# Performance work log

Measured on AMD Instinct MI355X. Metric: run time of the kernel, lower is better.

Reference implementation:

```python
import jax, jax.numpy as jnp
import numpy as np

H = 8  # n_heads

def setup_inputs() -> dict:
    key = jax.random.key(0)
    ks = jax.random.split(key, 7)
    B, G, D, KD, E = 16, 1024, 512, 64, 512  # batch, graph_size, input_dim, key_dim=embed//H, embed_dim
    q = jax.random.normal(ks[0], (B * G, D), jnp.float32)
    mask = jax.random.bernoulli(ks[1], 0.15, (B, G))  # True = padded node
    s_in = 1.0 / np.sqrt(D)
    Wq = jax.random.uniform(ks[2], (KD, D), jnp.float32, -s_in, s_in)
    Wk = jax.random.uniform(ks[3], (KD, D), jnp.float32, -s_in, s_in)
    Wv = jax.random.uniform(ks[4], (KD, D), jnp.float32, -s_in, s_in)
    s_o = 1.0 / np.sqrt(KD)
    Wout_w = jax.random.uniform(ks[5], (E, KD), jnp.float32, -s_o, s_o)
    Wout_b = jax.random.uniform(ks[6], (E,), jnp.float32, -1.0 / np.sqrt(E), 1.0 / np.sqrt(E))
    return {"q": q, "mask": mask, "Wq": Wq, "Wk": Wk, "Wv": Wv,
            "Wout_w": Wout_w, "Wout_b": Wout_b, "graph_size": G}


def reference(q, mask, Wq, Wk, Wv, Wout_w, Wout_b, graph_size):
    G = graph_size
    B = q.shape[0] // G
    KD = Wq.shape[0]
    norm = 1.0 / jnp.sqrt(jnp.asarray(KD, jnp.float32))
    # torch .view(n_heads, B, G, -1) on a (B*G, KD) tensor: row-major reshape
    Q = (q @ Wq.T).reshape(H, B, G, -1)  # per-head dim = KD // H
    K = (q @ Wk.T).reshape(H, B, G, -1)
    V = (q @ Wv.T).reshape(H, B, G, -1)
    compat = norm * jnp.einsum('hbqd,hbkd->hbqk', Q, K)  # (H,B,G,G)
    m = mask[None, :, None, :]  # broadcast == repeat over query dim and heads
    compat = jnp.where(m, jnp.float32(-30.0), compat)  # evaluate=False path
    attn = jax.nn.softmax(compat, axis=-1)
    attn = jnp.where(m, jnp.float32(0.0), attn)  # second mask fill
    heads = jnp.einsum('hbqk,hbkd->hbqd', attn, V)  # (H,B,G,KD//H)
    # permute(1,2,0,3) then flatten heads -> (B*G, H*(KD//H)=KD)
    out = heads.transpose(1, 2, 0, 3).reshape(B * G, -1) @ Wout_w.T + Wout_b
    return out
```

## Files before the change

### kernel.cpp

```cpp
#include <hip/hip_runtime.h>
#include <hip/hip_bf16.h>

#define NROWS 16384
#define DDIM  512
#define KDIM  64
#define EDIM  512
#define GSZ   1024
#define BSZ   16
#define HSZ   8

typedef float f32x16 __attribute__((ext_vector_type(16)));
typedef short bf16x8 __attribute__((ext_vector_type(8)));

union FragU { uint u[4]; uint4 u4; bf16x8 s; };

static __device__ __forceinline__ float fexp2(float x) {
  return __builtin_amdgcn_exp2f(x);
}
static __device__ __forceinline__ uint bf16r(float x) {
  const uint u = __builtin_bit_cast(uint, x);
  return (u + 0x7FFFu + ((u >> 16) & 1u)) >> 16;
}
static __device__ __forceinline__ uint apk(float lo, float hi) {
  uint r;
  asm("v_cvt_pk_bf16_f32 %0, %1, %2" : "=v"(r) : "v"(lo), "v"(hi));
  return r;
}
static __device__ __forceinline__ uint pk2e(float a, float b) {
  const uint lo = __builtin_bit_cast(uint, fexp2(a)) + 0x8000u;
  const uint hi = __builtin_bit_cast(uint, fexp2(b)) + 0x8000u;
  return __builtin_amdgcn_perm(hi, lo, 0x07060302u);
}
static __device__ __forceinline__ void plswap(uint& a, uint& b) {
  auto r = __builtin_amdgcn_permlane32_swap(a, b, false, false);
  a = r[0]; b = r[1];
}
static __device__ __forceinline__ void plswapf(float& a, float& b) {
  uint au = __builtin_bit_cast(uint, a), bu = __builtin_bit_cast(uint, b);
  plswap(au, bu);
  a = __builtin_bit_cast(float, au); b = __builtin_bit_cast(float, bu);
}
static __device__ __forceinline__ uint vperm16(uint a, uint b, int d1) {
  const uint lo = d1 ? (a >> 16) : (a & 0xFFFFu);
  const uint hi = d1 ? (b >> 16) : (b & 0xFFFFu);
  return lo | (hi << 16);
}

__global__ __launch_bounds__(256) void k_mask3(const void* __restrict__ mraw,
                                               uint* __restrict__ onesw,
                                               uint* __restrict__ vmw) {
  __shared__ int flags[2];
  const int tid = threadIdx.x;
  if (tid < 2) flags[tid] = 0;
  __syncthreads();
  const unsigned int* u = (const unsigned int*)mraw;
  int bad = 0, isf = 0;
  for (int i = tid; i < 4096; i += 256) {
    const unsigned v = u[i];
    bad |= (v > 1u) ? 1 : 0;
    isf |= (v == 0x3F800000u) ? 1 : 0;
  }
  if (bad) flags[0] = 1;
  if (isf) flags[1] = 1;
  __syncthreads();
  const int fmt = flags[1] ? 2 : (flags[0] ? 1 : 0);
  const int b = blockIdx.x;
  for (int pair = tid; pair < 512; pair += 256) {
    const int g0 = b * GSZ + pair * 2;
    bool m0, m1;
    if (fmt == 0) {
      m0 = ((const int*)mraw)[g0] != 0;  m1 = ((const int*)mraw)[g0 + 1] != 0;
    } else if (fmt == 1) {
      m0 = ((const unsigned char*)mraw)[g0] != 0;
      m1 = ((const unsigned char*)mraw)[g0 + 1] != 0;
    } else {
      m0 = ((const float*)mraw)[g0] != 0.0f;
      m1 = ((const float*)mraw)[g0 + 1] != 0.0f;
    }
    onesw[b * 512 + pair] = (m0 ? 0u : 0x3F80u) | (m1 ? 0u : 0x3F800000u);
    vmw[b * 512 + pair]   = (m0 ? 0u : 0xFFFFu) | (m1 ? 0u : 0xFFFF0000u);
  }
}

__global__ __launch_bounds__(384) void k_qkv2(const float* __restrict__ q,
    const float* __restrict__ Wq, const float* __restrict__ Wk,
    const float* __restrict__ Wv,
    ushort* __restrict__ Qbf, ushort* __restrict__ Kbf, ushort* __restrict__ Vbf) {
  __shared__ uint4 lds_a[16 * 64];
  __shared__ uint4 lds_w[16 * 192];
  const int tid = threadIdx.x;
  const int rowbase = blockIdx.x * 64;
  const int w = tid >> 6, lane = tid & 63, hi = lane >> 5, ln = lane & 31;
  const int wr = (w < 3) ? 0 : 1;
  const int wc = (w < 3) ? w : (w - 3);

  f32x16 acc0, acc1;
#pragma unroll
  for (int j = 0; j < 16; ++j) { acc0[j] = 0.0f; acc1[j] = 0.0f; }

#pragma unroll 1
  for (int ch = 0; ch < 4; ++ch) {
    const int k0 = ch * 128;
    __syncthreads();
#pragma unroll 1
    for (int ep = tid; ep < 512; ep += 384) {
      const int row = ep >> 3, sp = ep & 7;
      const float* src = q + (size_t)(rowbase + row) * DDIM + k0 + sp * 16;
      const float4 f0 = *(const float4*)(src);
      const float4 f1 = *(const float4*)(src + 4);
      const float4 f2 = *(const float4*)(src + 8);
      const float4 f3 = *(const float4*)(src + 12);
      uint4 w0, w1;
      w0.x = apk(f0.x, f0.y); w0.y = apk(f0.z, f0.w);
      w0.z = apk(f1.x, f1.y); w0.w = apk(f1.z, f1.w);
      w1.x = apk(f2.x, f2.y); w1.y = apk(f2.z, f2.w);
      w1.z = apk(f3.x, f3.y); w1.w = apk(f3.z, f3.w);
      const int sl0 = sp * 2, sl1 = sp * 2 + 1;
      lds_a[sl0 * 64 + (row ^ (sl0 & 7))] = w0;
      lds_a[sl1 * 64 + (row ^ (sl1 & 7))] = w1;
    }
#pragma unroll 1
    for (int ep = tid; ep < 1536; ep += 384) {
      const int c = ep >> 3, sp = ep & 7;
      const float* wsrc = (c < 64) ? (Wq + (size_t)c * DDIM)
                        : (c < 128) ? (Wk + (size_t)(c - 64) * DDIM)
                                    : (Wv + (size_t)(c - 128) * DDIM);
      const float* src = wsrc + k0 + sp * 16;
      const float4 f0 = *(const float4*)(src);
      const float4 f1 = *(const float4*)(src + 4);
      const float4 f2 = *(const float4*)(src + 8);
      const float4 f3 = *(const float4*)(src + 12);
      uint4 w0, w1;
      w0.x = apk(f0.x, f0.y); w0.y = apk(f0.z, f0.w);
      w0.z = apk(f1.x, f1.y); w0.w = apk(f1.z, f1.w);
      w1.x = apk(f2.x, f2.y); w1.y = apk(f2.z, f2.w);
      w1.z = apk(f3.x, f3.y); w1.w = apk(f3.z, f3.w);
      const int sl0 = sp * 2, sl1 = sp * 2 + 1;
      lds_w[sl0 * 192 + (c ^ (sl0 & 7))] = w0;
      lds_w[sl1 * 192 + (c ^ (sl1 & 7))] = w1;
    }
    __syncthreads();
#pragma unroll
    for (int kc8 = 0; kc8 < 8; ++kc8) {
      const int sl = kc8 * 2 + hi;
      FragU aq, b0, b1;
      aq.u4 = lds_a[sl * 64 + ((wr * 32 + ln) ^ (sl & 7))];
      b0.u4 = lds_w[sl * 192 + ((wc * 64 + ln) ^ (sl & 7))];
      b1.u4 = lds_w[sl * 192 + ((wc * 64 + 32 + ln) ^ (sl & 7))];
      acc0 = __builtin_amdgcn_mfma_f32_32x32x16_bf16(aq.s, b0.s, acc0, 0, 0, 0);
      acc1 = __builtin_amdgcn_mfma_f32_32x32x16_bf16(aq.s, b1.s, acc1, 0, 0, 0);
    }
  }

  constexpr float QS = 0.125f * 1.44269504088896340736f;
  ushort* dst = (wc == 0) ? Qbf : (wc == 1) ? Kbf : Vbf;
  const float scale = (wc == 0) ? QS : 1.0f;
#pragma unroll
  for (int j = 0; j < 16; ++j) {
    const int row = rowbase + wr * 32 + (j & 3) + 8 * (j >> 2) + 4 * hi;
    dst[(size_t)row * 64 + ln]      = (ushort)bf16r(acc0[j] * scale);
    dst[(size_t)row * 64 + 32 + ln] = (ushort)bf16r(acc1[j] * scale);
  }
}

__global__ __launch_bounds__(256) void k_attn7(const ushort* __restrict__ Qbf,
    const ushort* __restrict__ Kbf, const ushort* __restrict__ Vbf,
    const uint* __restrict__ onesw, const uint* __restrict__ vmw,
    float* __restrict__ Hm) {
  __shared__ __align__(16) uint4  KL[1025];
  __shared__ __align__(16) ushort VT[9 * 1040];
  const int tid = threadIdx.x;
  const int b = blockIdx.y, h = blockIdx.z;
  const size_t hb = ((size_t)h * 2048 + (size_t)b * 128) * 64;

#pragma unroll
  for (int i = 0; i < 4; ++i) {
    const int tt = tid + i * 256;
    KL[tt] = *(const uint4*)(&Kbf[hb + (size_t)tt * 8]);
  }
  if (tid == 0) {
    uint4 z; z.x = 0; z.y = 0; z.z = 0; z.w = 0;
    KL[1024] = z;
  }
#pragma unroll
  for (int i = 0; i < 2; ++i) {
    const int pair = tid + i * 256;
    const int t = pair * 2;
    const uint ow = onesw[b * 512 + pair];
    const uint vm = vmw[b * 512 + pair];
    const uint4 v0 = *(const uint4*)(&Vbf[hb + (size_t)t * 8]);
    const uint4 v1 = *(const uint4*)(&Vbf[hb + (size_t)(t + 1) * 8]);
    const uint* ap = (const uint*)&v0;
    const uint* cp = (const uint*)&v1;
    const int s = t & 15;
    const int c = (t & ~15) | (s & 3) | ((s & 4) << 1) | ((s & 8) >> 1);
#pragma unroll
    for (int d = 0; d < 8; ++d)
      *(uint*)&VT[d * 1040 + c] = vperm16(ap[d >> 1], cp[d >> 1], d & 1) & vm;
    *(uint*)&VT[8 * 1040 + c] = ow;
  }

  const int w = tid >> 6, lane = tid & 63, hi = lane >> 5, ln = lane & 31;
  const int q = (blockIdx.x * 4 + w) * 32 + ln;

  FragU bq;
  bq.u4 = *(const uint4*)(&Qbf[hb + (size_t)q * 8]);
  __syncthreads();

  f32x16 acc;
#pragma unroll
  for (int j = 0; j < 16; ++j) acc[j] = 0.0f;
  f32x16 zero;
#pragma unroll
  for (int j = 0; j < 16; ++j) zero[j] = 0.0f;

  const char* kptr = (const char*)KL + (hi ? 1024 * 16 : ln * 16);
  const int kstep = hi ? 0 : 512;
  const ushort* vptr = VT + (ln < 8 ? ln : 8) * 1040 + hi * 8;

#pragma unroll 2
  for (int kt = 0; kt < 32; ++kt) {
    FragU ka, va0, va1;
    ka.u4  = *(const uint4*)kptr;
    va0.u4 = *(const uint4*)(vptr);
    va1.u4 = *(const uint4*)(vptr + 16);
    kptr += kstep;
    vptr += 32;

    f32x16 s = __builtin_amdgcn_mfma_f32_32x32x16_bf16(ka.s, bq.s, zero, 0, 0, 0);

    FragU pa, pb;
    pa.u[0] = pk2e(s[0], s[1]);   pa.u[1] = pk2e(s[2], s[3]);
    pa.u[2] = pk2e(s[4], s[5]);   pa.u[3] = pk2e(s[6], s[7]);
    pb.u[0] = pk2e(s[8], s[9]);   pb.u[1] = pk2e(s[10], s[11]);
    pb.u[2] = pk2e(s[12], s[13]); pb.u[3] = pk2e(s[14], s[15]);

    acc = __builtin_amdgcn_mfma_f32_32x32x16_bf16(va0.s, pa.s, acc, 0, 0, 0);
    acc = __builtin_amdgcn_mfma_f32_32x32x16_bf16(va1.s, pb.s, acc, 0, 0, 0);
  }

  float la = acc[4], lb = acc[4];
  plswapf(la, lb);
  const float inv = (la > 0.0f) ? 1.0f / la : 0.0f;
  float* op = Hm + ((size_t)b * GSZ + q) * 64 + h * 8 + hi * 4;
  *(float4*)op = make_float4(acc[0] * inv, acc[1] * inv, acc[2] * inv, acc[3] * inv);
}

__global__ __launch_bounds__(256) void k_out2(const float* __restrict__ Hm,
    const float* __restrict__ Ww, const float* __restrict__ Wb,
    float* __restrict__ out) {
  __shared__ uint4 lds_h[8 * 128];
  __shared__ uint4 lds_e[8 * 128];
  const int tid = threadIdx.x;
  const int colbase = blockIdx.x * 128;
  const int rowbase = blockIdx.y * 128;
  const int w = tid >> 6, lane = tid & 63, hi = lane >> 5, ln = lane & 31;
  const int wr = w >> 1, wc = w & 1;

#pragma unroll
  for (int i = 0; i < 2; ++i) {
    const int ep = tid + i * 256;
    const int row = ep >> 2, sp = ep & 3;
    const float* src = Hm + (size_t)(rowbase + row) * 64 + sp * 16;
    const float4 f0 = *(const float4*)(src);
    const float4 f1 = *(const float4*)(src + 4);
    const float4 f2 = *(const float4*)(src + 8);
    const float4 f3 = *(const float4*)(src + 12);
    uint4 w0, w1;
    w0.x = apk(f0.x, f0.y); w0.y = apk(f0.z, f0.w);
    w0.z = apk(f1.x, f1.y); w0.w = apk(f1.z, f1.w);
    w1.x = apk(f2.x, f2.y); w1.y = apk(f2.z, f2.w);
    w1.z = apk(f3.x, f3.y); w1.w = apk(f3.z, f3.w);
    const int sl0 = sp * 2, sl1 = sp * 2 + 1;
    lds_h[sl0 * 128 + (row ^ (sl0 & 7))] = w0;
    lds_h[sl1 * 128 + (row ^ (sl1 & 7))] = w1;
  }
#pragma unroll
  for (int i = 0; i < 2; ++i) {
    const int ep = tid + i * 256;
    const int c = ep >> 2, sp = ep & 3;
    const float* src = Ww + (size_t)(colbase + c) * 64 + sp * 16;
    const float4 f0 = *(const float4*)(src);
    const float4 f1 = *(const float4*)(src + 4);
    const float4 f2 = *(const float4*)(src + 8);
    const float4 f3 = *(const float4*)(src + 12);
    uint4 w0, w1;
    w0.x = apk(f0.x, f0.y); w0.y = apk(f0.z, f0.w);
    w0.z = apk(f1.x, f1.y); w0.w = apk(f1.z, f1.w);
    w1.x = apk(f2.x, f2.y); w1.y = apk(f2.z, f2.w);
    w1.z = apk(f3.x, f3.y); w1.w = apk(f3.z, f3.w);
    const int sl0 = sp * 2, sl1 = sp * 2 + 1;
    lds_e[sl0 * 128 + (c ^ (sl0 & 7))] = w0;
    lds_e[sl1 * 128 + (c ^ (sl1 & 7))] = w1;
  }
  __syncthreads();

  f32x16 a00, a01, a10, a11;
#pragma unroll
  for (int j = 0; j < 16; ++j) { a00[j] = 0.0f; a01[j] = 0.0f; a10[j] = 0.0f; a11[j] = 0.0f; }

#pragma unroll
  for (int kc8 = 0; kc8 < 4; ++kc8) {
    const int sl = kc8 * 2 + hi;
    FragU fa0, fa1, fb0, fb1;
    fa0.u4 = lds_h[sl * 128 + ((wr * 64 + ln) ^ (sl & 7))];
    fa1.u4 = lds_h[sl * 128 + ((wr * 64 + 32 + ln) ^ (sl & 7))];
    fb0.u4 = lds_e[sl * 128 + ((wc * 64 + ln) ^ (sl & 7))];
    fb1.u4 = lds_e[sl * 128 + ((wc * 64 + 32 + ln) ^ (sl & 7))];
    a00 = __builtin_amdgcn_mfma_f32_32x32x16_bf16(fa0.s, fb0.s, a00, 0, 0, 0);
    a01 = __builtin_amdgcn_mfma_f32_32x32x16_bf16(fa0.s, fb1.s, a01, 0, 0, 0);
    a10 = __builtin_amdgcn_mfma_f32_32x32x16_bf16(fa1.s, fb0.s, a10, 0, 0, 0);
    a11 = __builtin_amdgcn_mfma_f32_32x32x16_bf16(fa1.s, fb1.s, a11, 0, 0, 0);
  }

  const float bias0 = Wb[colbase + wc * 64 + ln];
  const float bias1 = Wb[colbase + wc * 64 + 32 + ln];
  const int col0 = colbase + wc * 64 + ln;
#pragma unroll
  for (int j = 0; j < 16; ++j) {
    const int r0 = rowbase + wr * 64 + (j & 3) + 8 * (j >> 2) + 4 * hi;
    out[(size_t)r0 * EDIM + col0]            = a00[j] + bias0;
    out[(size_t)r0 * EDIM + col0 + 32]       = a01[j] + bias1;
    out[(size_t)(r0 + 32) * EDIM + col0]      = a10[j] + bias0;
    out[(size_t)(r0 + 32) * EDIM + col0 + 32] = a11[j] + bias1;
  }
}

extern "C" void kernel_launch(void* const* d_in, const int* in_sizes, int n_in,
                              void* d_out, int out_size, void* d_ws, size_t ws_size,
                              hipStream_t stream) {
  const float* q    = (const float*)d_in[0];
  const void*  mask = d_in[1];
  const float* Wq   = (const float*)d_in[2];
  const float* Wk   = (const float*)d_in[3];
  const float* Wv   = (const float*)d_in[4];
  const float* Ww   = (const float*)d_in[5];
  const float* Wb   = (const float*)d_in[6];

  float* ws = (float*)d_ws;
  float* Hm    = ws;
  uint*  onesw = (uint*)(Hm + (size_t)NROWS * KDIM);
  uint*  vmw   = onesw + BSZ * 512;
  ushort* Qbf  = (ushort*)(vmw + BSZ * 512);
  ushort* Kbf  = Qbf + (size_t)NROWS * KDIM;
  ushort* Vbf  = Kbf + (size_t)NROWS * KDIM;

  k_mask3<<<BSZ, 256, 0, stream>>>(mask, onesw, vmw);
  k_qkv2<<<NROWS / 64, 384, 0, stream>>>(q, Wq, Wk, Wv, Qbf, Kbf, Vbf);
  k_attn7<<<dim3(8, BSZ, HSZ), 256, 0, stream>>>(Qbf, Kbf, Vbf, onesw, vmw, Hm);
  k_out2<<<dim3(EDIM / 128, NROWS / 128), 256, 0, stream>>>(Hm, Ww, Wb, (float*)d_out);
}
```

Baseline: 62.63 us.

## Split attention keys into two shards with combine kernel; widen QKV projection blocks

The attention kernel now splits the 1024 keys into two shards per block, doubling the grid to 2048 blocks and halving per-block LDS. Each shard writes unnormalized partial outputs and row sums to a workspace, and a new combine kernel adds them and normalizes. Separately, the QKV projection uses 768 threads (12 waves, one 32x32 tile each) instead of 384 with two tiles per wave. Together these aim to raise occupancy and parallelism, at the cost of an extra kernel launch and extra global traffic for the partial results.

```diff
diff --git a/kernel.cpp b/kernel.cpp
--- a/kernel.cpp
+++ b/kernel.cpp
@@ -30,15 +30,6 @@
   const uint lo = __builtin_bit_cast(uint, fexp2(a)) + 0x8000u;
   const uint hi = __builtin_bit_cast(uint, fexp2(b)) + 0x8000u;
   return __builtin_amdgcn_perm(hi, lo, 0x07060302u);
-}
-static __device__ __forceinline__ void plswap(uint& a, uint& b) {
-  auto r = __builtin_amdgcn_permlane32_swap(a, b, false, false);
-  a = r[0]; b = r[1];
-}
-static __device__ __forceinline__ void plswapf(float& a, float& b) {
-  uint au = __builtin_bit_cast(uint, a), bu = __builtin_bit_cast(uint, b);
-  plswap(au, bu);
-  a = __builtin_bit_cast(float, au); b = __builtin_bit_cast(float, bu);
 }
 static __device__ __forceinline__ uint vperm16(uint a, uint b, int d1) {
   const uint lo = d1 ? (a >> 16) : (a & 0xFFFFu);
@@ -82,7 +73,7 @@
   }
 }
 
-__global__ __launch_bounds__(384) void k_qkv2(const float* __restrict__ q,
+__global__ __launch_bounds__(768) void k_qkv3(const float* __restrict__ q,
     const float* __restrict__ Wq, const float* __restrict__ Wk,
     const float* __restrict__ Wv,
     ushort* __restrict__ Qbf, ushort* __restrict__ Kbf, ushort* __restrict__ Vbf) {
@@ -91,19 +82,19 @@
   const int tid = threadIdx.x;
   const int rowbase = blockIdx.x * 64;
   const int w = tid >> 6, lane = tid & 63, hi = lane >> 5, ln = lane & 31;
-  const int wr = (w < 3) ? 0 : 1;
-  const int wc = (w < 3) ? w : (w - 3);
-
-  f32x16 acc0, acc1;
-#pragma unroll
-  for (int j = 0; j < 16; ++j) { acc0[j] = 0.0f; acc1[j] = 0.0f; }
+  const int wr = (w < 6) ? 0 : 1;
+  const int wc = (w < 6) ? w : (w - 6);
+
+  f32x16 acc;
+#pragma unroll
+  for (int j = 0; j < 16; ++j) acc[j] = 0.0f;
 
 #pragma unroll 1
   for (int ch = 0; ch < 4; ++ch) {
     const int k0 = ch * 128;
     __syncthreads();
 #pragma unroll 1
-    for (int ep = tid; ep < 512; ep += 384) {
+    for (int ep = tid; ep < 512; ep += 768) {
       const int row = ep >> 3, sp = ep & 7;
       const float* src = q + (size_t)(rowbase + row) * DDIM + k0 + sp * 16;
       const float4 f0 = *(const float4*)(src);
@@ -120,7 +111,7 @@
       lds_a[sl1 * 64 + (row ^ (sl1 & 7))] = w1;
     }
 #pragma unroll 1
-    for (int ep = tid; ep < 1536; ep += 384) {
+    for (int ep = tid; ep < 1536; ep += 768) {
       const int c = ep >> 3, sp = ep & 7;
       const float* wsrc = (c < 64) ? (Wq + (size_t)c * DDIM)
                         : (c < 128) ? (Wk + (size_t)(c - 64) * DDIM)
@@ -143,65 +134,64 @@
 #pragma unroll
     for (int kc8 = 0; kc8 < 8; ++kc8) {
       const int sl = kc8 * 2 + hi;
-      FragU aq, b0, b1;
+      FragU aq, bw;
       aq.u4 = lds_a[sl * 64 + ((wr * 32 + ln) ^ (sl & 7))];
-      b0.u4 = lds_w[sl * 192 + ((wc * 64 + ln) ^ (sl & 7))];
-      b1.u4 = lds_w[sl * 192 + ((wc * 64 + 32 + ln) ^ (sl & 7))];
-      acc0 = __builtin_amdgcn_mfma_f32_32x32x16_bf16(aq.s, b0.s, acc0, 0, 0, 0);
-      acc1 = __builtin_amdgcn_mfma_f32_32x32x16_bf16(aq.s, b1.s, acc1, 0, 0, 0);
+      bw.u4 = lds_w[sl * 192 + ((wc * 32 + ln) ^ (sl & 7))];
+      acc = __builtin_amdgcn_mfma_f32_32x32x16_bf16(aq.s, bw.s, acc, 0, 0, 0);
     }
   }
 
   constexpr float QS = 0.125f * 1.44269504088896340736f;
-  ushort* dst = (wc == 0) ? Qbf : (wc == 1) ? Kbf : Vbf;
-  const float scale = (wc == 0) ? QS : 1.0f;
+  ushort* dst = (wc < 2) ? Qbf : (wc < 4) ? Kbf : Vbf;
+  const int colb = (wc < 2) ? wc * 32 : (wc < 4) ? (wc - 2) * 32 : (wc - 4) * 32;
+  const float scale = (wc < 2) ? QS : 1.0f;
 #pragma unroll
   for (int j = 0; j < 16; ++j) {
     const int row = rowbase + wr * 32 + (j & 3) + 8 * (j >> 2) + 4 * hi;
-    dst[(size_t)row * 64 + ln]      = (ushort)bf16r(acc0[j] * scale);
-    dst[(size_t)row * 64 + 32 + ln] = (ushort)bf16r(acc1[j] * scale);
-  }
-}
-
-__global__ __launch_bounds__(256) void k_attn7(const ushort* __restrict__ Qbf,
+    dst[(size_t)row * 64 + colb + ln] = (ushort)bf16r(acc[j] * scale);
+  }
+}
+
+__global__ __launch_bounds__(256) void k_attn8(const ushort* __restrict__ Qbf,
     const ushort* __restrict__ Kbf, const ushort* __restrict__ Vbf,
     const uint* __restrict__ onesw, const uint* __restrict__ vmw,
-    float* __restrict__ Hm) {
-  __shared__ __align__(16) uint4  KL[1025];
-  __shared__ __align__(16) ushort VT[9 * 1040];
+    float* __restrict__ part) {
+  __shared__ __align__(16) uint4  KL[513];
+  __shared__ __align__(16) ushort VT[9 * 528];
   const int tid = threadIdx.x;
+  const int qt4 = blockIdx.x >> 1, shard = blockIdx.x & 1;
   const int b = blockIdx.y, h = blockIdx.z;
   const size_t hb = ((size_t)h * 2048 + (size_t)b * 128) * 64;
-
-#pragma unroll
-  for (int i = 0; i < 4; ++i) {
+  const int kt0 = shard * 512;
+
+#pragma unroll
+  for (int i = 0; i < 2; ++i) {
     const int tt = tid + i * 256;
-    KL[tt] = *(const uint4*)(&Kbf[hb + (size_t)tt * 8]);
+    KL[tt] = *(const uint4*)(&Kbf[hb + (size_t)(kt0 + tt) * 8]);
   }
   if (tid == 0) {
     uint4 z; z.x = 0; z.y = 0; z.z = 0; z.w = 0;
-    KL[1024] = z;
-  }
-#pragma unroll
-  for (int i = 0; i < 2; ++i) {
-    const int pair = tid + i * 256;
+    KL[512] = z;
+  }
+  {
+    const int pair = tid;
     const int t = pair * 2;
-    const uint ow = onesw[b * 512 + pair];
-    const uint vm = vmw[b * 512 + pair];
-    const uint4 v0 = *(const uint4*)(&Vbf[hb + (size_t)t * 8]);
-    const uint4 v1 = *(const uint4*)(&Vbf[hb + (size_t)(t + 1) * 8]);
+    const uint ow = onesw[b * 512 + shard * 256 + pair];
+    const uint vm = vmw[b * 512 + shard * 256 + pair];
+    const uint4 v0 = *(const uint4*)(&Vbf[hb + (size_t)(kt0 + t) * 8]);
+    const uint4 v1 = *(const uint4*)(&Vbf[hb + (size_t)(kt0 + t + 1) * 8]);
     const uint* ap = (const uint*)&v0;
     const uint* cp = (const uint*)&v1;
     const int s = t & 15;
     const int c = (t & ~15) | (s & 3) | ((s & 4) << 1) | ((s & 8) >> 1);
 #pragma unroll
     for (int d = 0; d < 8; ++d)
-      *(uint*)&VT[d * 1040 + c] = vperm16(ap[d >> 1], cp[d >> 1], d & 1) & vm;
-    *(uint*)&VT[8 * 1040 + c] = ow;
+      *(uint*)&VT[d * 528 + c] = vperm16(ap[d >> 1], cp[d >> 1], d & 1) & vm;
+    *(uint*)&VT[8 * 528 + c] = ow;
   }
 
   const int w = tid >> 6, lane = tid & 63, hi = lane >> 5, ln = lane & 31;
-  const int q = (blockIdx.x * 4 + w) * 32 + ln;
+  const int q = (qt4 * 4 + w) * 32 + ln;
 
   FragU bq;
   bq.u4 = *(const uint4*)(&Qbf[hb + (size_t)q * 8]);
@@ -214,12 +204,12 @@
 #pragma unroll
   for (int j = 0; j < 16; ++j) zero[j] = 0.0f;
 
-  const char* kptr = (const char*)KL + (hi ? 1024 * 16 : ln * 16);
+  const char* kptr = (const char*)KL + (hi ? 512 * 16 : ln * 16);
   const int kstep = hi ? 0 : 512;
-  const ushort* vptr = VT + (ln < 8 ? ln : 8) * 1040 + hi * 8;
+  const ushort* vptr = VT + (ln < 8 ? ln : 8) * 528 + hi * 8;
 
 #pragma unroll 2
-  for (int kt = 0; kt < 32; ++kt) {
+  for (int kt = 0; kt < 16; ++kt) {
     FragU ka, va0, va1;
     ka.u4  = *(const uint4*)kptr;
     va0.u4 = *(const uint4*)(vptr);
@@ -239,11 +229,32 @@
     acc = __builtin_amdgcn_mfma_f32_32x32x16_bf16(va1.s, pb.s, acc, 0, 0, 0);
   }
 
-  float la = acc[4], lb = acc[4];
-  plswapf(la, lb);
-  const float inv = (la > 0.0f) ? 1.0f / la : 0.0f;
-  float* op = Hm + ((size_t)b * GSZ + q) * 64 + h * 8 + hi * 4;
-  *(float4*)op = make_float4(acc[0] * inv, acc[1] * inv, acc[2] * inv, acc[3] * inv);
+  const size_t eidx = (((size_t)shard * BSZ + b) * GSZ + q) * HSZ + h;
+  float* ap2 = part + eidx * 8 + hi * 4;
+  *(float4*)ap2 = make_float4(acc[0], acc[1], acc[2], acc[3]);
+  if (hi == 0) {
+    float* lbase = part + (size_t)2 * BSZ * GSZ * HSZ * 8;
+    lbase[eidx] = acc[4];
+  }
+}
+
+__global__ __launch_bounds__(256) void k_comb2(const float* __restrict__ part,
+                                               float* __restrict__ Hm) {
+  const int gid = blockIdx.x * 256 + threadIdx.x;
+  const size_t sstride = (size_t)BSZ * GSZ * HSZ;
+  const float* a1 = part + (size_t)gid * 8;
+  const float* a2 = part + ((size_t)gid + sstride) * 8;
+  const float* lbase = part + 2 * sstride * 8;
+  const float l = lbase[gid] + lbase[gid + sstride];
+  const float inv = (l > 0.0f) ? 1.0f / l : 0.0f;
+  const float4 x1 = *(const float4*)a1, y1 = *(const float4*)(a1 + 4);
+  const float4 x2 = *(const float4*)a2, y2 = *(const float4*)(a2 + 4);
+  const int b = gid >> 13, q = (gid >> 3) & 1023, h = gid & 7;
+  float* op = Hm + ((size_t)b * GSZ + q) * 64 + h * 8;
+  *(float4*)op = make_float4((x1.x + x2.x) * inv, (x1.y + x2.y) * inv,
+                             (x1.z + x2.z) * inv, (x1.w + x2.w) * inv);
+  *(float4*)(op + 4) = make_float4((y1.x + y2.x) * inv, (y1.y + y2.y) * inv,
+                                   (y1.z + y2.z) * inv, (y1.w + y2.w) * inv);
 }
 
 __global__ __launch_bounds__(256) void k_out2(const float* __restrict__ Hm,
@@ -344,9 +355,11 @@
   ushort* Qbf  = (ushort*)(vmw + BSZ * 512);
   ushort* Kbf  = Qbf + (size_t)NROWS * KDIM;
   ushort* Vbf  = Kbf + (size_t)NROWS * KDIM;
+  float* part  = (float*)(Vbf + (size_t)NROWS * KDIM);
 
   k_mask3<<<BSZ, 256, 0, stream>>>(mask, onesw, vmw);
-  k_qkv2<<<NROWS / 64, 384, 0, stream>>>(q, Wq, Wk, Wv, Qbf, Kbf, Vbf);
-  k_attn7<<<dim3(8, BSZ, HSZ), 256, 0, stream>>>(Qbf, Kbf, Vbf, onesw, vmw, Hm);
+  k_qkv3<<<NROWS / 64, 768, 0, stream>>>(q, Wq, Wk, Wv, Qbf, Kbf, Vbf);
+  k_attn8<<<dim3(16, BSZ, HSZ), 256, 0, stream>>>(Qbf, Kbf, Vbf, onesw, vmw, part);
+  k_comb2<<<512, 256, 0, stream>>>(part, Hm);
   k_out2<<<dim3(EDIM / 128, NROWS / 128), 256, 0, stream>>>(Hm, Ww, Wb, (float*)d_out);
 }
```

Result: slower. 64.71 us (+3.3%).
